# Kernel tuning notes

Measured on AMD Instinct MI355X. Metric: run time of the kernel, lower is better.

The kernel has to match this reference:

```python
import jax, jax.numpy as jnp
import numpy as np

N, E, G = 50000, 800000, 128
F_IN, H, NHID, C = 310, 128, 64, 2  # H = 2*nhid
NEG_SLOPE = 0.2


def setup_inputs() -> dict:
    key = jax.random.key(0)
    ks = jax.random.split(key, 16)
    def lin(k, fan_in, shape):
        return (jax.random.normal(k, shape, jnp.float32) / np.sqrt(fan_in)).astype(jnp.float32)
    return {
        "x": jax.random.normal(ks[0], (N, F_IN), jnp.float32),
        "edge_index": jax.random.randint(ks[1], (2, E), 0, N, dtype=jnp.int32),
        "batch": jnp.sort(jax.random.randint(ks[2], (N,), 0, G, dtype=jnp.int32)),
        "W1": lin(ks[3], F_IN, (F_IN, H)),
        "a_src1": lin(ks[4], H, (H,)),
        "a_dst1": lin(ks[5], H, (H,)),
        "b1": jnp.zeros((H,), jnp.float32),
        "W2": lin(ks[6], H, (H, H)),
        "a_src2": lin(ks[7], H, (H,)),
        "a_dst2": lin(ks[8], H, (H,)),
        "b2": jnp.zeros((H,), jnp.float32),
        "fc1_w": lin(ks[9], H, (H, NHID)),
        "fc1_b": jnp.zeros((NHID,), jnp.float32),
        "fc2_w": lin(ks[10], NHID, (NHID, C)),
        "fc2_b": jnp.zeros((C,), jnp.float32),
    }


def _gat(x, src, dst, W, a_src, a_dst, b):
    # PyG GATConv, heads=1: h = xW; e_ij = LeakyReLU(a_src.h_j + a_dst.h_i)
    h = x @ W                               # [N, H]
    asrc = h @ a_src                        # [N]
    adst = h @ a_dst                        # [N]
    e = jax.nn.leaky_relu(asrc[src] + adst[dst], NEG_SLOPE)  # [E']
    # segment softmax over incoming edges of each target node
    m = jax.ops.segment_max(e, dst, num_segments=N)
    ex = jnp.exp(e - m[dst])
    s = jax.ops.segment_sum(ex, dst, num_segments=N)
    w = ex / s[dst]                         # [E']
    out = jax.ops.segment_sum(h[src] * w[:, None], dst, num_segments=N)
    return out + b


def reference(x, edge_index, batch, W1, a_src1, a_dst1, b1,
              W2, a_src2, a_dst2, b2, fc1_w, fc1_b, fc2_w, fc2_b):
    # add self loops (GATConv default add_self_loops=True)
    ar = jnp.arange(N, dtype=edge_index.dtype)
    src = jnp.concatenate([edge_index[0], ar])
    dst = jnp.concatenate([edge_index[1], ar])

    h = jax.nn.selu(_gat(x, src, dst, W1, a_src1, a_dst1, b1))
    h = jax.nn.selu(_gat(h, src, dst, W2, a_src2, a_dst2, b2))

    # global mean pool over graphs
    summed = jax.ops.segment_sum(h, batch, num_segments=G)          # [G, H]
    cnt = jax.ops.segment_sum(jnp.ones((N,), h.dtype), batch, num_segments=G)
    pooled = jax.nn.selu(summed / jnp.maximum(cnt, 1.0)[:, None])

    z = jax.nn.selu(pooled @ fc1_w + fc1_b)  # dropout is identity in eval
    logits = z @ fc2_w + fc2_b
    return jax.nn.log_softmax(logits, axis=-1)
```

## Files before the change

### kernel.cpp

```cpp
#include <hip/hip_runtime.h>
#include <hip/hip_bf16.h>
#include <math.h>

#define NN 50000
#define NE 800000
#define NET (NE + NN)
#define FIN 310
#define HD 128
#define NHID 64
#define NCLS 2
#define NG 128
#define NEG_SLOPE 0.2f
#define KP1 320
#define KP2 128

#define SLOTS 64
#define NPART 8
#define PART_SZ (NN / NPART)
#define EPB 4096
#define NSLICE ((NET + EPB - 1) / EPB)
#define SSPLIT 104
#define NSC_MIX (SSPLIT * 8)
#define NSC_PRE ((NSLICE - SSPLIT) * 8)
#define GB1 ((NN + 63) / 64)
#define CXB ((NN * 40 + 255) / 256)

#define SELU_SCALE 1.0507009873554804934193349852946f
#define SELU_ALPHA 1.6732632423543772848170429916717f

typedef short bf16x8 __attribute__((ext_vector_type(8)));
typedef float f32x4 __attribute__((ext_vector_type(4)));

__device__ __forceinline__ float selu(float x) {
    return SELU_SCALE * (x > 0.f ? x : SELU_ALPHA * (__expf(x) - 1.f));
}
__device__ __forceinline__ float lrelu(float x) {
    return x > 0.f ? x : NEG_SLOPE * x;
}
__device__ __forceinline__ unsigned short f2bf(float f) {
    unsigned int u = __float_as_uint(f);
    u = (u + 0x7fffu + ((u >> 16) & 1u)) >> 16;
    return (unsigned short)u;
}
__device__ __forceinline__ float bf2f(unsigned short b) {
    return __uint_as_float(((unsigned int)b) << 16);
}


__global__ void k_castW(const float* __restrict__ W1, const float* __restrict__ W2,
                        unsigned short* __restrict__ W1p, unsigned short* __restrict__ W2p,
                        int* __restrict__ cursor) {
    int i = blockIdx.x * blockDim.x + threadIdx.x;
    if (i < NN) cursor[i] = 0;
    const int N1 = HD * KP1;
    if (i < N1) {
        int n = i / KP1, k = i % KP1;
        unsigned short v = (k < FIN) ? f2bf(W1[(size_t)k * HD + n]) : (unsigned short)0;
        W1p[((k >> 3) * HD + n) * 8 + (k & 7)] = v;
    } else {
        int j = i - N1;
        if (j < HD * KP2) {
            int n = j / KP2, k = j % KP2;
            W2p[((k >> 3) * HD + n) * 8 + (k & 7)] = f2bf(W2[(size_t)k * HD + n]);
        }
    }
}


__device__ __forceinline__ void scatter_body(int slice, const int* __restrict__ ei,
                                             int* __restrict__ cursor,
                                             unsigned short* __restrict__ slots,
                                             int part) {
    int lo = part * PART_SZ;
    int base = slice * EPB + threadIdx.x;
#pragma unroll
    for (int k = 0; k < EPB / 256; ++k) {
        int i = base + k * 256;
        if (i >= NET) break;
        int d = (i < NE) ? ei[NE + i] : (i - NE);
        if ((unsigned)(d - lo) < (unsigned)PART_SZ) {
            int s = (i < NE) ? ei[i] : d;
            int pos = atomicAdd(&cursor[d], 1) & (SLOTS - 1);
            slots[(size_t)d * SLOTS + pos] = (unsigned short)s;
        }
    }
}


#define RGEMM_EPILOGUE                                                         \
    int gr_base = r0 + w * 16 + quad * 4;                                      \
    _Pragma("unroll")                                                          \
    for (int r = 0; r < 4; ++r) {                                              \
        int gr = gr_base + r;                                                  \
        if (gr < M) {                                                          \
            _Pragma("unroll")                                                  \
            for (int nt = 0; nt < 8; ++nt)                                     \
                C[(size_t)gr * HD + nt * 16 + l16] = f2bf(acc[nt][r]);         \
        }                                                                      \
    }                                                                          \
    _Pragma("unroll")                                                          \
    for (int r = 0; r < 4; ++r) {                                              \
        float s1 = 0.f, s2 = 0.f;                                              \
        _Pragma("unroll")                                                      \
        for (int nt = 0; nt < 8; ++nt) {                                       \
            int c = nt * 16 + l16;                                             \
            float v = acc[nt][r];                                              \
            s1 += v * a_src[c];                                                \
            s2 += v * a_dst[c];                                                \
        }                                                                      \
        _Pragma("unroll")                                                      \
        for (int off = 1; off < 16; off <<= 1) {                               \
            s1 += __shfl_xor(s1, off);                                         \
            s2 += __shfl_xor(s2, off);                                         \
        }                                                                      \
        int gr = gr_base + r;                                                  \
        if (l16 == 0 && gr < M) { asrcp[gr] = s1; adstp[gr] = s2; }            \
    }


template <int KP>
__device__ __forceinline__ void gemm_rows(const unsigned short* __restrict__ A,
                                          const unsigned short* __restrict__ Bp,
                                          unsigned short* __restrict__ C,
                                          float* __restrict__ asrcp,
                                          float* __restrict__ adstp,
                                          const float* __restrict__ a_src,
                                          const float* __restrict__ a_dst,
                                          int M) {
    int t = threadIdx.x;
    int lane = t & 63, w = t >> 6;
    int quad = lane >> 4, l16 = lane & 15;
    int r0 = blockIdx.x * 64;

    int grow = r0 + w * 16 + l16;
    int arow = min(grow, M - 1);
    const unsigned short* aptr = A + (size_t)arow * KP + quad * 8;

    f32x4 acc[8] = {};
#pragma unroll
    for (int k0 = 0; k0 < KP; k0 += 32) {
        bf16x8 af = *(const bf16x8*)(aptr + k0);
        const unsigned short* bbase = Bp + ((size_t)(k0 >> 3) + quad) * (HD * 8) + l16 * 8;
#pragma unroll
        for (int nt = 0; nt < 8; ++nt) {
            bf16x8 bfr = *(const bf16x8*)(bbase + nt * 128);
            acc[nt] = __builtin_amdgcn_mfma_f32_16x16x32_bf16(af, bfr, acc[nt], 0, 0, 0);
        }
    }
    RGEMM_EPILOGUE
}


__global__ __launch_bounds__(256) void k_mix(const float* __restrict__ x,
                                             unsigned short* __restrict__ xb,
                                             const int* __restrict__ ei,
                                             int* __restrict__ cursor,
                                             unsigned short* __restrict__ slots) {
    if (blockIdx.x < NSC_MIX) {
        int part = (blockIdx.x + 2) & 7;
        scatter_body(blockIdx.x >> 3, ei, cursor, slots, part);
        return;
    }
    int j = (blockIdx.x - NSC_MIX) * 256 + threadIdx.x;
    int row = j / 40;
    if (row >= NN) return;
    int c0 = (j - row * 40) * 8;
    const float* xp = x + (size_t)row * FIN + c0;
    union { bf16x8 v; unsigned short u[8]; } o;
    if (c0 + 8 <= FIN) {
        float2 f0 = *(const float2*)(xp + 0);
        float2 f1 = *(const float2*)(xp + 2);
        float2 f2 = *(const float2*)(xp + 4);
        float2 f3 = *(const float2*)(xp + 6);
        o.u[0] = f2bf(f0.x); o.u[1] = f2bf(f0.y);
        o.u[2] = f2bf(f1.x); o.u[3] = f2bf(f1.y);
        o.u[4] = f2bf(f2.x); o.u[5] = f2bf(f2.y);
        o.u[6] = f2bf(f3.x); o.u[7] = f2bf(f3.y);
    } else {
#pragma unroll
        for (int q = 0; q < 8; ++q)
            o.u[q] = (c0 + q < FIN) ? f2bf(xp[q]) : (unsigned short)0;
    }
    *(bf16x8*)(xb + (size_t)row * KP1 + c0) = o.v;
}


__global__ __launch_bounds__(256) void k_pre(const unsigned short* __restrict__ xb,
                                             const unsigned short* __restrict__ Bp,
                                             unsigned short* __restrict__ C,
                                             float* __restrict__ asrcp,
                                             float* __restrict__ adstp,
                                             const float* __restrict__ a_src,
                                             const float* __restrict__ a_dst,
                                             int M,
                                             const int* __restrict__ ei,
                                             int* __restrict__ cursor,
                                             unsigned short* __restrict__ slots) {
    if (blockIdx.x >= GB1) {
        int b = blockIdx.x - GB1;
        int part = (blockIdx.x + 2) & 7;
        scatter_body(SSPLIT + (b >> 3), ei, cursor, slots, part);
        return;
    }
    gemm_rows<KP1>(xb, Bp, C, asrcp, adstp, a_src, a_dst, M);
}


__global__ __launch_bounds__(256) void k_gemm2(const unsigned short* __restrict__ A,
                                               const unsigned short* __restrict__ Bp,
                                               unsigned short* __restrict__ C,
                                               float* __restrict__ asrcp,
                                               float* __restrict__ adstp,
                                               const float* __restrict__ a_src,
                                               const float* __restrict__ a_dst,
                                               int M) {
    gemm_rows<KP2>(A, Bp, C, asrcp, adstp, a_src, a_dst, M);
}


__global__ __launch_bounds__(256) void k_gat(const unsigned short* __restrict__ h,
                                             const float* __restrict__ asrc,
                                             const float* __restrict__ adst,
                                             const int* __restrict__ degv,
                                             const unsigned short* __restrict__ slots,
                                             const float* __restrict__ bias,
                                             unsigned short* __restrict__ out) {
    int node = blockIdx.x * 4 + (threadIdx.x >> 6);
    int lane = threadIdx.x & 63;
    if (node >= NN) return;
    int g = lane >> 4, cl = lane & 15;
    int deg = degv[node];
    float adsti = adst[node];

    float2 acc2[4] = {};

    int cnt = min(deg, SLOTS);
    int s_c = 0; float p_c = 0.f;
    if (lane < cnt) {
        s_c = slots[(size_t)node * SLOTS + lane];
        p_c = __expf(lrelu(asrc[s_c] + adsti));
    }
    float den_l = p_c;
    int nt = (cnt + 3) >> 2;
    for (int t = 0; t < nt; t += 4) {
        float pv[4]; uint4 hv[4];
#pragma unroll
        for (int u = 0; u < 4; ++u) {
            int tt = t + u;
            bool valid = tt < nt;
            int e = (4 * tt + g) & 63;
            int s = __shfl(s_c, e);
            float p = __shfl(p_c, e);
            int sa = valid ? s : 0;
            pv[u] = valid ? p : 0.f;
            hv[u] = *(const uint4*)(h + (size_t)sa * HD + cl * 8);
        }
#pragma unroll
        for (int u = 0; u < 4; ++u) {
            float p = pv[u];
            unsigned int w0 = hv[u].x, w1 = hv[u].y, w2 = hv[u].z, w3 = hv[u].w;
            acc2[0].x += p * __uint_as_float(w0 << 16);
            acc2[0].y += p * __uint_as_float(w0 & 0xffff0000u);
            acc2[1].x += p * __uint_as_float(w1 << 16);
            acc2[1].y += p * __uint_as_float(w1 & 0xffff0000u);
            acc2[2].x += p * __uint_as_float(w2 << 16);
            acc2[2].y += p * __uint_as_float(w2 & 0xffff0000u);
            acc2[3].x += p * __uint_as_float(w3 << 16);
            acc2[3].y += p * __uint_as_float(w3 & 0xffff0000u);
        }
    }
#pragma unroll
    for (int k = 0; k < 4; ++k) {
        acc2[k].x += __shfl_xor(acc2[k].x, 16);
        acc2[k].y += __shfl_xor(acc2[k].y, 16);
        acc2[k].x += __shfl_xor(acc2[k].x, 32);
        acc2[k].y += __shfl_xor(acc2[k].y, 32);
    }
#pragma unroll
    for (int off = 32; off; off >>= 1)
        den_l += __shfl_xor(den_l, off);

    if (g == 0) {
        float inv = 1.f / den_l;
        int c0 = cl * 8;
        float4 b0 = *(const float4*)(bias + c0);
        float4 b1 = *(const float4*)(bias + c0 + 4);
        float v0 = selu(acc2[0].x * inv + b0.x);
        float v1 = selu(acc2[0].y * inv + b0.y);
        float v2 = selu(acc2[1].x * inv + b0.z);
        float v3 = selu(acc2[1].y * inv + b0.w);
        float v4 = selu(acc2[2].x * inv + b1.x);
        float v5 = selu(acc2[2].y * inv + b1.y);
        float v6 = selu(acc2[3].x * inv + b1.z);
        float v7 = selu(acc2[3].y * inv + b1.w);
        uint4 pk;
        pk.x = (unsigned int)f2bf(v0) | ((unsigned int)f2bf(v1) << 16);
        pk.y = (unsigned int)f2bf(v2) | ((unsigned int)f2bf(v3) << 16);
        pk.z = (unsigned int)f2bf(v4) | ((unsigned int)f2bf(v5) << 16);
        pk.w = (unsigned int)f2bf(v6) | ((unsigned int)f2bf(v7) << 16);
        *(uint4*)(out + (size_t)node * HD + c0) = pk;
    }
}


__device__ __forceinline__ int lower_bound_i(const int* a, int n, int key) {
    int lo = 0, hi = n;
    while (lo < hi) {
        int mid = (lo + hi) >> 1;
        if (a[mid] < key) lo = mid + 1; else hi = mid;
    }
    return lo;
}

__global__ __launch_bounds__(512) void k_poolfc(const unsigned short* __restrict__ x,
                                                const int* __restrict__ batch,
                                                const float* __restrict__ w1,
                                                const float* __restrict__ b1,
                                                const float* __restrict__ w2,
                                                const float* __restrict__ b2,
                                                float* __restrict__ out) {
    int g = blockIdx.x;
    int t = threadIdx.x;
    __shared__ int lo_s, hi_s;
    __shared__ float red[512];
    __shared__ float pooled_s[128];
    if (t == 0) {
        lo_s = lower_bound_i(batch, NN, g);
        hi_s = lower_bound_i(batch, NN, g + 1);
    }
    __syncthreads();
    int lo = lo_s, hi = hi_s;
    float acc = 0.f;
    for (int n = lo + (t >> 7); n < hi; n += 4)
        acc += bf2f(x[(size_t)n * HD + (t & 127)]);
    red[t] = acc;
    __syncthreads();
    if (t < 128) {
        float v = red[t] + red[t + 128] + red[t + 256] + red[t + 384];
        pooled_s[t] = selu(v / fmaxf((float)(hi - lo), 1.f));
    }
    __syncthreads();
    if (t < 64) {
        float z = 0.f;
#pragma unroll 8
        for (int k = 0; k < HD; ++k) z += pooled_s[k] * w1[k * NHID + t];
        z = selu(z + b1[t]);
        float p0 = z * w2[t * NCLS + 0];
        float p1 = z * w2[t * NCLS + 1];
        for (int off = 32; off; off >>= 1) {
            p0 += __shfl_down(p0, off);
            p1 += __shfl_down(p1, off);
        }
        if (t == 0) {
            float l0 = p0 + b2[0], l1 = p1 + b2[1];
            float m = fmaxf(l0, l1);
            float lse = m + __logf(__expf(l0 - m) + __expf(l1 - m));
            out[g * NCLS + 0] = l0 - lse;
            out[g * NCLS + 1] = l1 - lse;
        }
    }
}


static inline size_t align_up(size_t v, size_t a) { return (v + a - 1) / a * a; }

extern "C" void kernel_launch(void* const* d_in, const int* in_sizes, int n_in,
                              void* d_out, int out_size, void* d_ws, size_t ws_size,
                              hipStream_t stream) {
    const float* x      = (const float*)d_in[0];
    const int*   ei     = (const int*)d_in[1];
    const int*   batch  = (const int*)d_in[2];
    const float* W1     = (const float*)d_in[3];
    const float* a_src1 = (const float*)d_in[4];
    const float* a_dst1 = (const float*)d_in[5];
    const float* b1     = (const float*)d_in[6];
    const float* W2     = (const float*)d_in[7];
    const float* a_src2 = (const float*)d_in[8];
    const float* a_dst2 = (const float*)d_in[9];
    const float* b2     = (const float*)d_in[10];
    const float* fc1_w  = (const float*)d_in[11];
    const float* fc1_b  = (const float*)d_in[12];
    const float* fc2_w  = (const float*)d_in[13];
    const float* fc2_b  = (const float*)d_in[14];
    float* out = (float*)d_out;

    char* ws = (char*)d_ws;
    size_t off = 0;
    unsigned short* h1  = (unsigned short*)(ws + off); off = align_up(off + (size_t)NN * HD * 2, 256);
    unsigned short* o1  = (unsigned short*)(ws + off); off = align_up(off + (size_t)NN * HD * 2, 256);
    float* asrc = (float*)(ws + off); off = align_up(off + (size_t)NN * 4, 256);
    float* adst = (float*)(ws + off); off = align_up(off + (size_t)NN * 4, 256);
    int* cursor = (int*)(ws + off);   off = align_up(off + (size_t)NN * 4, 256);
    unsigned short* slots = (unsigned short*)(ws + off); off = align_up(off + (size_t)NN * SLOTS * 2, 256);
    unsigned short* W1p = (unsigned short*)(ws + off); off = align_up(off + (size_t)HD * KP1 * 2, 256);
    unsigned short* W2p = (unsigned short*)(ws + off); off = align_up(off + (size_t)HD * KP2 * 2, 256);
    unsigned short* xb  = (unsigned short*)(ws + off); off = align_up(off + (size_t)NN * KP1 * 2, 256);
    (void)ws_size;

    k_castW<<<(HD * (KP1 + KP2) + 255) / 256, 256, 0, stream>>>(W1, W2, W1p, W2p, cursor);

    k_mix<<<NSC_MIX + CXB, 256, 0, stream>>>(x, xb, ei, cursor, slots);

    k_pre<<<GB1 + NSC_PRE, 256, 0, stream>>>(xb, W1p, h1, asrc, adst, a_src1, a_dst1, NN,
                                             ei, cursor, slots);

    k_gat<<<(NN + 3) / 4, 256, 0, stream>>>(h1, asrc, adst, cursor, slots, b1, o1);

    k_gemm2<<<GB1, 256, 0, stream>>>(o1, W2p, h1, asrc, adst, a_src2, a_dst2, NN);
    k_gat<<<(NN + 3) / 4, 256, 0, stream>>>(h1, asrc, adst, cursor, slots, b2, o1);

    k_poolfc<<<NG, 512, 0, stream>>>(o1, batch, fc1_w, fc1_b, fc2_w, fc2_b, out);
}
```

Measured before the change: 298.1 us.

## Fuse layer-1 GAT aggregation with layer-2 GEMM and merge x cast into weight prep

Merges the x-to-bf16 conversion into the weight-packing kernel and moves all edge scattering into the GEMM1 kernel. Layer-1 GAT aggregation is fused with the layer-2 MFMA GEMM through a shared-memory tile, so the intermediate activations never round-trip through global memory. Layer-2 attention scalars go to separate buffers to avoid a race with in-flight reads. This removes a launch and a global write/read of the hidden state, but the fused kernel has far fewer blocks (64 nodes each), which may reduce latency hiding in the gather. The fused aggregation also drops the max subtraction in the softmax and caps degree at the slot count.

```diff
diff --git a/kernel.cpp b/kernel.cpp
--- a/kernel.cpp
+++ b/kernel.cpp
@@ -19,9 +19,7 @@
 #define PART_SZ (NN / NPART)
 #define EPB 4096
 #define NSLICE ((NET + EPB - 1) / EPB)
-#define SSPLIT 104
-#define NSC_MIX (SSPLIT * 8)
-#define NSC_PRE ((NSLICE - SSPLIT) * 8)
+#define NSC (NSLICE * NPART)
 #define GB1 ((NN + 63) / 64)
 #define CXB ((NN * 40 + 255) / 256)
 
@@ -47,9 +45,10 @@
 }
 
 
-__global__ void k_castW(const float* __restrict__ W1, const float* __restrict__ W2,
-                        unsigned short* __restrict__ W1p, unsigned short* __restrict__ W2p,
-                        int* __restrict__ cursor) {
+__global__ void k_castWX(const float* __restrict__ W1, const float* __restrict__ W2,
+                         const float* __restrict__ x,
+                         unsigned short* __restrict__ W1p, unsigned short* __restrict__ W2p,
+                         unsigned short* __restrict__ xb, int* __restrict__ cursor) {
     int i = blockIdx.x * blockDim.x + threadIdx.x;
     if (i < NN) cursor[i] = 0;
     const int N1 = HD * KP1;
@@ -57,12 +56,31 @@
         int n = i / KP1, k = i % KP1;
         unsigned short v = (k < FIN) ? f2bf(W1[(size_t)k * HD + n]) : (unsigned short)0;
         W1p[((k >> 3) * HD + n) * 8 + (k & 7)] = v;
-    } else {
+    } else if (i - N1 < HD * KP2) {
         int j = i - N1;
-        if (j < HD * KP2) {
-            int n = j / KP2, k = j % KP2;
-            W2p[((k >> 3) * HD + n) * 8 + (k & 7)] = f2bf(W2[(size_t)k * HD + n]);
-        }
+        int n = j / KP2, k = j % KP2;
+        W2p[((k >> 3) * HD + n) * 8 + (k & 7)] = f2bf(W2[(size_t)k * HD + n]);
+    }
+    int row = i / 40;
+    if (row < NN) {
+        int c0 = (i - row * 40) * 8;
+        const float* xp = x + (size_t)row * FIN + c0;
+        union { bf16x8 v; unsigned short u[8]; } o;
+        if (c0 + 8 <= FIN) {
+            float2 f0 = *(const float2*)(xp + 0);
+            float2 f1 = *(const float2*)(xp + 2);
+            float2 f2 = *(const float2*)(xp + 4);
+            float2 f3 = *(const float2*)(xp + 6);
+            o.u[0] = f2bf(f0.x); o.u[1] = f2bf(f0.y);
+            o.u[2] = f2bf(f1.x); o.u[3] = f2bf(f1.y);
+            o.u[4] = f2bf(f2.x); o.u[5] = f2bf(f2.y);
+            o.u[6] = f2bf(f3.x); o.u[7] = f2bf(f3.y);
+        } else {
+#pragma unroll
+            for (int q = 0; q < 8; ++q)
+                o.u[q] = (c0 + q < FIN) ? f2bf(xp[q]) : (unsigned short)0;
+        }
+        *(bf16x8*)(xb + (size_t)row * KP1 + c0) = o.v;
     }
 }
 
@@ -151,40 +169,6 @@
 }
 
 
-__global__ __launch_bounds__(256) void k_mix(const float* __restrict__ x,
-                                             unsigned short* __restrict__ xb,
-                                             const int* __restrict__ ei,
-                                             int* __restrict__ cursor,
-                                             unsigned short* __restrict__ slots) {
-    if (blockIdx.x < NSC_MIX) {
-        int part = (blockIdx.x + 2) & 7;
-        scatter_body(blockIdx.x >> 3, ei, cursor, slots, part);
-        return;
-    }
-    int j = (blockIdx.x - NSC_MIX) * 256 + threadIdx.x;
-    int row = j / 40;
-    if (row >= NN) return;
-    int c0 = (j - row * 40) * 8;
-    const float* xp = x + (size_t)row * FIN + c0;
-    union { bf16x8 v; unsigned short u[8]; } o;
-    if (c0 + 8 <= FIN) {
-        float2 f0 = *(const float2*)(xp + 0);
-        float2 f1 = *(const float2*)(xp + 2);
-        float2 f2 = *(const float2*)(xp + 4);
-        float2 f3 = *(const float2*)(xp + 6);
-        o.u[0] = f2bf(f0.x); o.u[1] = f2bf(f0.y);
-        o.u[2] = f2bf(f1.x); o.u[3] = f2bf(f1.y);
-        o.u[4] = f2bf(f2.x); o.u[5] = f2bf(f2.y);
-        o.u[6] = f2bf(f3.x); o.u[7] = f2bf(f3.y);
-    } else {
-#pragma unroll
-        for (int q = 0; q < 8; ++q)
-            o.u[q] = (c0 + q < FIN) ? f2bf(xp[q]) : (unsigned short)0;
-    }
-    *(bf16x8*)(xb + (size_t)row * KP1 + c0) = o.v;
-}
-
-
 __global__ __launch_bounds__(256) void k_pre(const unsigned short* __restrict__ xb,
                                              const unsigned short* __restrict__ Bp,
                                              unsigned short* __restrict__ C,
@@ -199,14 +183,19 @@
     if (blockIdx.x >= GB1) {
         int b = blockIdx.x - GB1;
         int part = (blockIdx.x + 2) & 7;
-        scatter_body(SSPLIT + (b >> 3), ei, cursor, slots, part);
+        scatter_body(b >> 3, ei, cursor, slots, part);
         return;
     }
     gemm_rows<KP1>(xb, Bp, C, asrcp, adstp, a_src, a_dst, M);
 }
 
 
-__global__ __launch_bounds__(256) void k_gemm2(const unsigned short* __restrict__ A,
+__global__ __launch_bounds__(256) void k_gatg2(const unsigned short* __restrict__ h,
+                                               const float* __restrict__ asrc,
+                                               const float* __restrict__ adst,
+                                               const int* __restrict__ degv,
+                                               const unsigned short* __restrict__ slots,
+                                               const float* __restrict__ bias,
                                                const unsigned short* __restrict__ Bp,
                                                unsigned short* __restrict__ C,
                                                float* __restrict__ asrcp,
@@ -214,7 +203,102 @@
                                                const float* __restrict__ a_src,
                                                const float* __restrict__ a_dst,
                                                int M) {
-    gemm_rows<KP2>(A, Bp, C, asrcp, adstp, a_src, a_dst, M);
+    __shared__ unsigned short Al[64][136];
+    int t = threadIdx.x;
+    int n0 = blockIdx.x * 64;
+    {
+        int wv = t >> 6;
+        int lane = t & 63;
+        int g = lane >> 4, l = lane & 15;
+        int gid = wv * 4 + g;
+
+        for (int it = 0; it < 4; ++it) {
+            int node = n0 + it * 16 + gid;
+            bool vn = node < NN;
+            int cnt = vn ? min(degv[node], SLOTS) : 0;
+            float adsti = vn ? adst[node] : 0.f;
+            int s_c[4]; float p_c[4];
+#pragma unroll
+            for (int j = 0; j < 4; ++j) {
+                int e = l + 16 * j;
+                bool v = e < cnt;
+                int s = v ? (int)slots[(size_t)node * SLOTS + e] : 0;
+                s_c[j] = s;
+                p_c[j] = v ? __expf(lrelu(asrc[s] + adsti)) : 0.f;
+            }
+            float den = p_c[0] + p_c[1] + p_c[2] + p_c[3];
+#pragma unroll
+            for (int off = 1; off < 16; off <<= 1) den += __shfl_xor(den, off, 16);
+
+            int mc = cnt;
+            mc = max(mc, __shfl_xor(mc, 16));
+            mc = max(mc, __shfl_xor(mc, 32));
+
+            float2 acc2[4] = {};
+#pragma unroll
+            for (int j = 0; j < 4; ++j) {
+                if (16 * j < mc) {
+                    int quads = (min(mc - 16 * j, 16) + 3) >> 2;
+                    for (int q = 0; q < quads; ++q) {
+                        float pv[4]; uint4 hv[4];
+#pragma unroll
+                        for (int u = 0; u < 4; ++u) {
+                            int e = q * 4 + u;
+                            int s = __shfl(s_c[j], e, 16);
+                            pv[u] = __shfl(p_c[j], e, 16);
+                            hv[u] = *(const uint4*)(h + (size_t)s * HD + l * 8);
+                        }
+#pragma unroll
+                        for (int u = 0; u < 4; ++u) {
+                            float p = pv[u];
+                            unsigned int w0 = hv[u].x, w1 = hv[u].y, w2 = hv[u].z, w3 = hv[u].w;
+                            acc2[0].x += p * __uint_as_float(w0 << 16);
+                            acc2[0].y += p * __uint_as_float(w0 & 0xffff0000u);
+                            acc2[1].x += p * __uint_as_float(w1 << 16);
+                            acc2[1].y += p * __uint_as_float(w1 & 0xffff0000u);
+                            acc2[2].x += p * __uint_as_float(w2 << 16);
+                            acc2[2].y += p * __uint_as_float(w2 & 0xffff0000u);
+                            acc2[3].x += p * __uint_as_float(w3 << 16);
+                            acc2[3].y += p * __uint_as_float(w3 & 0xffff0000u);
+                        }
+                    }
+                }
+            }
+            float inv = (den > 0.f) ? 1.f / den : 0.f;
+            int c0 = l * 8;
+            float4 b0 = *(const float4*)(bias + c0);
+            float4 b1v = *(const float4*)(bias + c0 + 4);
+            union { bf16x8 v; unsigned short u[8]; } o;
+            o.u[0] = f2bf(selu(acc2[0].x * inv + b0.x));
+            o.u[1] = f2bf(selu(acc2[0].y * inv + b0.y));
+            o.u[2] = f2bf(selu(acc2[1].x * inv + b0.z));
+            o.u[3] = f2bf(selu(acc2[1].y * inv + b0.w));
+            o.u[4] = f2bf(selu(acc2[2].x * inv + b1v.x));
+            o.u[5] = f2bf(selu(acc2[2].y * inv + b1v.y));
+            o.u[6] = f2bf(selu(acc2[3].x * inv + b1v.z));
+            o.u[7] = f2bf(selu(acc2[3].y * inv + b1v.w));
+            *(bf16x8*)&Al[it * 16 + gid][c0] = o.v;
+        }
+    }
+    __syncthreads();
+    {
+        int lane = t & 63, w = t >> 6;
+        int quad = lane >> 4, l16 = lane & 15;
+        int r0 = blockIdx.x * 64;
+        int arow = w * 16 + l16;
+        f32x4 acc[8] = {};
+#pragma unroll
+        for (int k0 = 0; k0 < KP2; k0 += 32) {
+            bf16x8 af = *(const bf16x8*)&Al[arow][quad * 8 + k0];
+            const unsigned short* bbase = Bp + ((size_t)(k0 >> 3) + quad) * (HD * 8) + l16 * 8;
+#pragma unroll
+            for (int nt = 0; nt < 8; ++nt) {
+                bf16x8 bfr = *(const bf16x8*)(bbase + nt * 128);
+                acc[nt] = __builtin_amdgcn_mfma_f32_16x16x32_bf16(af, bfr, acc[nt], 0, 0, 0);
+            }
+        }
+        RGEMM_EPILOGUE
+    }
 }
 
 
@@ -390,6 +474,8 @@
     unsigned short* o1  = (unsigned short*)(ws + off); off = align_up(off + (size_t)NN * HD * 2, 256);
     float* asrc = (float*)(ws + off); off = align_up(off + (size_t)NN * 4, 256);
     float* adst = (float*)(ws + off); off = align_up(off + (size_t)NN * 4, 256);
+    float* asrc2 = (float*)(ws + off); off = align_up(off + (size_t)NN * 4, 256);
+    float* adst2 = (float*)(ws + off); off = align_up(off + (size_t)NN * 4, 256);
     int* cursor = (int*)(ws + off);   off = align_up(off + (size_t)NN * 4, 256);
     unsigned short* slots = (unsigned short*)(ws + off); off = align_up(off + (size_t)NN * SLOTS * 2, 256);
     unsigned short* W1p = (unsigned short*)(ws + off); off = align_up(off + (size_t)HD * KP1 * 2, 256);
@@ -397,17 +483,15 @@
     unsigned short* xb  = (unsigned short*)(ws + off); off = align_up(off + (size_t)NN * KP1 * 2, 256);
     (void)ws_size;
 
-    k_castW<<<(HD * (KP1 + KP2) + 255) / 256, 256, 0, stream>>>(W1, W2, W1p, W2p, cursor);
-
-    k_mix<<<NSC_MIX + CXB, 256, 0, stream>>>(x, xb, ei, cursor, slots);
-
-    k_pre<<<GB1 + NSC_PRE, 256, 0, stream>>>(xb, W1p, h1, asrc, adst, a_src1, a_dst1, NN,
-                                             ei, cursor, slots);
-
-    k_gat<<<(NN + 3) / 4, 256, 0, stream>>>(h1, asrc, adst, cursor, slots, b1, o1);
-
-    k_gemm2<<<GB1, 256, 0, stream>>>(o1, W2p, h1, asrc, adst, a_src2, a_dst2, NN);
-    k_gat<<<(NN + 3) / 4, 256, 0, stream>>>(h1, asrc, adst, cursor, slots, b2, o1);
-
-    k_poolfc<<<NG, 512, 0, stream>>>(o1, batch, fc1_w, fc1_b, fc2_w, fc2_b, out);
-}
+    k_castWX<<<CXB, 256, 0, stream>>>(W1, W2, x, W1p, W2p, xb, cursor);
+
+    k_pre<<<GB1 + NSC, 256, 0, stream>>>(xb, W1p, h1, asrc, adst, a_src1, a_dst1, NN,
+                                         ei, cursor, slots);
+
+    k_gatg2<<<GB1, 256, 0, stream>>>(h1, asrc, adst, cursor, slots, b1,
+                                     W2p, o1, asrc2, adst2, a_src2, a_dst2, NN);
+
+    k_gat<<<(NN + 3) / 4, 256, 0, stream>>>(o1, asrc2, adst2, cursor, slots, b2, h1);
+
+    k_poolfc<<<NG, 512, 0, stream>>>(h1, batch, fc1_w, fc1_b, fc2_w, fc2_b, out);
+}
```

Measured after the change: 300.1 us. About the same (+0.7%).
